# Optimization experiments

Hardware: AMD Instinct MI355X
Metric: run time of the kernel (lower is better)

## Reference

```python
import jax, jax.numpy as jnp
import numpy as np

N_ANGLES = 8
K = 15


def setup_inputs() -> dict:
    key = jax.random.key(0)
    k1, k2, k3 = jax.random.split(key, 3)
    N, Cin, Cout = 2048, 16, 32
    NA = N_ANGLES * N
    x = jax.random.normal(k1, (N, Cin), dtype=jnp.float32)
    # scaled so spectral radius ~1 (like a normalized Laplacian) to keep the
    # Chebyshev recurrence numerically bounded
    Ls = jax.random.normal(k2, (NA, NA), dtype=jnp.float32) / np.float32(np.sqrt(NA))
    fan = N_ANGLES * Cin + Cout  # xavier_uniform bound
    bound = np.float32(np.sqrt(6.0 / fan))
    weight = jax.random.uniform(k3, (K, N_ANGLES * Cin, Cout), dtype=jnp.float32,
                                minval=-bound, maxval=bound)
    bias = jnp.zeros((Cout,), dtype=jnp.float32)
    return {"x": x, "Ls": Ls, "weight": weight, "bias": bias}


def _proj(T, Wk, N, Cin):
    # T: [n_angles*N, Cin] -> [N, n_angles*Cin] @ Wk -> [N, Cout]
    return T.reshape(N_ANGLES, N, Cin).transpose(1, 0, 2).reshape(N, N_ANGLES * Cin) @ Wk


def reference(x, Ls, weight, bias):
    N, Cin = x.shape
    Tx0 = jnp.tile(x, (N_ANGLES, 1))            # [nA*N, Cin]
    out = _proj(Tx0, weight[0], N, Cin)          # [N, Cout]
    Tx1 = Ls @ Tx0
    out = out + _proj(Tx1, weight[1], N, Cin)
    for k in range(2, K):
        Tx2 = 2.0 * (Ls @ Tx1) - Tx0
        out = out + _proj(Tx2, weight[k], N, Cin)
        Tx0, Tx1 = Tx1, Tx2
    return out + bias
```

## Files before the change

### kernel.cpp

```cpp
#include <hip/hip_runtime.h>
#include <hip/hip_fp16.h>

#define NA   16384
#define NN   2048
#define CIN  16
#define COUT 32
#define NANG 8
#define KCH  15
#define NSTEP  512
#define CHUNK  4
#define NCHUNK (NSTEP / CHUNK)
#define NPANEL 1024

#define TSCALE_INV 0.03125f
#define TSCALE     32.0f


typedef _Float16 f16x8 __attribute__((ext_vector_type(8)));
typedef _Float16 f16x4 __attribute__((ext_vector_type(4)));
typedef float    f32x4 __attribute__((ext_vector_type(4)));

__global__ __launch_bounds__(256) void k_tile_t(const float* __restrict__ x,
                                                float* __restrict__ T32,
                                                _Float16* __restrict__ Tsw) {
    int tid = blockIdx.x * 256 + threadIdx.x;
    if (tid >= 8 * 64 * 64) return;
    const int s  = tid >> 12;
    const int st = (tid >> 6) & 63;
    const int l  = tid & 63;
    const int ch = l & 15;
    const int c2 = ((l >> 4) << 3) + (st << 5);
    f16x8 h;
    float v[8];
    #pragma unroll
    for (int e = 0; e < 8; ++e) {
        v[e] = x[(c2 + e) * CIN + ch];
        h[e] = (_Float16)(v[e] * TSCALE_INV);
    }
    float* d = T32 + (size_t)ch * NA + s * (NA / 8) + c2;
    *(float4*)(d)     = make_float4(v[0], v[1], v[2], v[3]);
    *(float4*)(d + 4) = make_float4(v[4], v[5], v[6], v[7]);
    *(f16x8*)(Tsw + (size_t)tid * 8) = h;
}

#define LOADCHUNK(BUF, PC)                                                   \
    _Pragma("unroll")                                                        \
    for (int u = 0; u < CHUNK; ++u) {                                        \
        const int st = (PC) * CHUNK + u;                                     \
        if (CONV) {                                                          \
            f32x4 f0 = __builtin_nontemporal_load((const f32x4*)(aF + (size_t)st * 32));     \
            f32x4 f1 = __builtin_nontemporal_load((const f32x4*)(aF + (size_t)st * 32 + 4)); \
            f16x8 h;                                                         \
            h[0] = (_Float16)f0[0]; h[1] = (_Float16)f0[1];                  \
            h[2] = (_Float16)f0[2]; h[3] = (_Float16)f0[3];                  \
            h[4] = (_Float16)f1[0]; h[5] = (_Float16)f1[1];                  \
            h[6] = (_Float16)f1[2]; h[7] = (_Float16)f1[3];                  \
            __builtin_nontemporal_store(h, (f16x8*)(aW + (size_t)st * 512)); \
            A[BUF][u] = h;                                                   \
        } else {                                                             \
            A[BUF][u] = __builtin_nontemporal_load((const f16x8*)(aP + (size_t)st * 512));   \
        }                                                                    \
        B[BUF][u] = *(const f16x8*)(bP + (size_t)st * 512);                  \
    }

template<int CONV, int REV>
__global__ __launch_bounds__(256)
void k_sweep(const float* __restrict__ Ls,
             _Float16* __restrict__ Lsw,
             const _Float16* __restrict__ Tsw,
             const float* __restrict__ Tp,
             float* __restrict__ Tn,
             _Float16* __restrict__ Tswn,
             float alpha, float beta) {
    constexpr int DEPTH = CONV ? 2 : 4;
    static_assert(NCHUNK % 2 == 0 && NCHUNK % 4 == 0,
                  "tail chunk would replay stale buffer");
    const int w   = threadIdx.x >> 6;
    const int l   = threadIdx.x & 63;
    const int bid = REV ? ((int)gridDim.x - 1 - (int)blockIdx.x) : (int)blockIdx.x;
    const int p   = bid * 4 + w;
    const int rc  = l & 15;
    const int kg  = l >> 4;

    const size_t aoff = (size_t)p * (NSTEP * 512) + (size_t)l * 8;
    const _Float16* aP = Lsw + aoff;
    _Float16*       aW = Lsw + aoff;
    const float*    aF = Ls + (size_t)(p * 16 + rc) * NA + kg * 8;
    const _Float16* bP = Tsw + (size_t)l * 8;

    f32x4 acc = {0.f, 0.f, 0.f, 0.f};
    f16x8 A[DEPTH][CHUNK], B[DEPTH][CHUNK];

    LOADCHUNK(0, 0);
    if (DEPTH >= 3) { LOADCHUNK(1 & (DEPTH - 1), 1); }
    if (DEPTH >= 4) { LOADCHUNK(2 & (DEPTH - 1), 2); }

    #pragma unroll 1
    for (int cc = 0; cc < NCHUNK; cc += DEPTH) {
        #pragma unroll
        for (int d = 0; d < DEPTH; ++d) {
            const int pf = cc + d + DEPTH - 1;
            if (pf < NCHUNK) { LOADCHUNK((d + DEPTH - 1) % DEPTH, pf); }
            #pragma unroll
            for (int u = 0; u < CHUNK; ++u)
                acc = __builtin_amdgcn_mfma_f32_16x16x32_f16(A[d][u], B[d][u],
                                                             acc, 0, 0, 0);
        }
    }

    const size_t tb = (size_t)rc * NA + (size_t)p * 16 + kg * 4;
    float4 tp4 = make_float4(0.f, 0.f, 0.f, 0.f);
    if (beta != 0.f) tp4 = *(const float4*)(Tp + tb);
    const float v0 = alpha * acc[0] + beta * tp4.x;
    const float v1 = alpha * acc[1] + beta * tp4.y;
    const float v2 = alpha * acc[2] + beta * tp4.z;
    const float v3 = alpha * acc[3] + beta * tp4.w;
    *(float4*)(Tn + tb) = make_float4(v0, v1, v2, v3);
    const int c0 = p * 16 + kg * 4;
    const size_t tf = ((size_t)(c0 >> 5) * 64 + ((c0 >> 3) & 3) * 16 + rc) * 8
                      + (c0 & 7);
    f16x4 h;
    h[0] = (_Float16)(v0 * TSCALE_INV); h[1] = (_Float16)(v1 * TSCALE_INV);
    h[2] = (_Float16)(v2 * TSCALE_INV); h[3] = (_Float16)(v3 * TSCALE_INV);
    *(f16x4*)(Tswn + tf) = h;
}

__global__ __launch_bounds__(256) void k_proj_t(const float* __restrict__ Tt,
                                                const float* __restrict__ W,
                                                const float* __restrict__ bias,
                                                float* __restrict__ out, int add) {
    int idx = blockIdx.x * 256 + threadIdx.x;
    if (idx >= NN * COUT) return;
    const int n  = idx >> 5;
    const int co = idx & 31;
    float s = add ? out[idx] : bias[co];
    #pragma unroll
    for (int a = 0; a < NANG; ++a)
        #pragma unroll
        for (int ci = 0; ci < CIN; ++ci)
            s = fmaf(Tt[(size_t)ci * NA + a * NN + n],
                     W[(size_t)(a * CIN + ci) * COUT + co], s);
    out[idx] = s;
}

extern "C" void kernel_launch(void* const* d_in, const int* in_sizes, int n_in,
                              void* d_out, int out_size, void* d_ws, size_t ws_size,
                              hipStream_t stream) {
    const float* x    = (const float*)d_in[0];
    const float* Ls   = (const float*)d_in[1];
    const float* W    = (const float*)d_in[2];
    const float* bias = (const float*)d_in[3];
    float* out = (float*)d_out;

    char* wsb = (char*)d_ws;
    _Float16* Lsw = (_Float16*)wsb;
    float* T32base = (float*)(wsb + (size_t)NA * NA * sizeof(_Float16));
    const size_t TSZ = (size_t)CIN * NA;
    float* T32[3] = { T32base, T32base + TSZ, T32base + 2 * TSZ };
    _Float16* Tswbase = (_Float16*)(T32base + 3 * TSZ);
    _Float16* Tsw[3] = { Tswbase, Tswbase + TSZ, Tswbase + 2 * TSZ };

    const int WSTRIDE = (NANG * CIN) * COUT;
    const int PGRID = (NN * COUT + 255) / 256;
    const int FGRID = (8 * 64 * 64) / 256;
    const int SGRID = NPANEL / 4;

    k_tile_t<<<FGRID, 256, 0, stream>>>(x, T32[0], Tsw[0]);
    k_proj_t<<<PGRID, 256, 0, stream>>>(T32[0], W, bias, out, 0);

    k_sweep<1, 0><<<SGRID, 256, 0, stream>>>(Ls, Lsw, Tsw[0], T32[0],
                                             T32[1], Tsw[1], TSCALE, 0.f);
    k_proj_t<<<PGRID, 256, 0, stream>>>(T32[1], W + WSTRIDE, bias, out, 1);

    int prev = 0, cur = 1;
    for (int k = 2; k < KCH; ++k) {
        int nxt = 3 - cur - prev;
        if (k & 1)
            k_sweep<0, 0><<<SGRID, 256, 0, stream>>>(Ls, Lsw, Tsw[cur], T32[prev],
                                                     T32[nxt], Tsw[nxt],
                                                     2.0f * TSCALE, -1.f);
        else
            k_sweep<0, 1><<<SGRID, 256, 0, stream>>>(Ls, Lsw, Tsw[cur], T32[prev],
                                                     T32[nxt], Tsw[nxt],
                                                     2.0f * TSCALE, -1.f);
        k_proj_t<<<PGRID, 256, 0, stream>>>(T32[nxt], W + (size_t)k * WSTRIDE,
                                            bias, out, 1);
        prev = cur; cur = nxt;
    }
}
```

Baseline: 2.015 ms.

## Fuse previous-step projection into Chebyshev sweep kernel as extra blocks

The projection for step k-1 now runs as extra thread blocks inside the sweep kernel for step k, instead of as a separate launch after each sweep. This removes one kernel launch and its serialization gap per Chebyshev step, and lets the small projection overlap with the memory-bound Ls sweep. The last projection still runs as a standalone launch. The projection blocks are placed first in the grid, so they may delay sweep blocks slightly, and they add register pressure to the sweep kernel.

```diff
diff --git a/kernel.cpp b/kernel.cpp
--- a/kernel.cpp
+++ b/kernel.cpp
@@ -11,6 +11,8 @@
 #define CHUNK  4
 #define NCHUNK (NSTEP / CHUNK)
 #define NPANEL 1024
+#define PGRID  ((NN * COUT) / 256)
+#define SGRID  (NPANEL / 4)
 
 #define TSCALE_INV 0.03125f
 #define TSCALE     32.0f
@@ -41,6 +43,23 @@
     *(float4*)(d)     = make_float4(v[0], v[1], v[2], v[3]);
     *(float4*)(d + 4) = make_float4(v[4], v[5], v[6], v[7]);
     *(f16x8*)(Tsw + (size_t)tid * 8) = h;
+}
+
+__device__ __forceinline__ void proj_body(const float* __restrict__ Tt,
+                                          const float* __restrict__ W,
+                                          const float* __restrict__ bias,
+                                          float* __restrict__ out, int add,
+                                          int idx) {
+    const int n  = idx >> 5;
+    const int co = idx & 31;
+    float s = add ? out[idx] : bias[co];
+    #pragma unroll
+    for (int a = 0; a < NANG; ++a)
+        #pragma unroll
+        for (int ci = 0; ci < CIN; ++ci)
+            s = fmaf(Tt[(size_t)ci * NA + a * NN + n],
+                     W[(size_t)(a * CIN + ci) * COUT + co], s);
+    out[idx] = s;
 }
 
 #define LOADCHUNK(BUF, PC)                                                   \
@@ -71,16 +90,26 @@
              const float* __restrict__ Tp,
              float* __restrict__ Tn,
              _Float16* __restrict__ Tswn,
-             float alpha, float beta) {
+             float alpha, float beta,
+             const float* __restrict__ Tproj,
+             const float* __restrict__ Wk,
+             const float* __restrict__ bias,
+             float* __restrict__ out, int add) {
+    if (blockIdx.x < PGRID) {
+        proj_body(Tproj, Wk, bias, out, add,
+                  (int)blockIdx.x * 256 + (int)threadIdx.x);
+        return;
+    }
     constexpr int DEPTH = CONV ? 2 : 4;
     static_assert(NCHUNK % 2 == 0 && NCHUNK % 4 == 0,
                   "tail chunk would replay stale buffer");
-    const int w   = threadIdx.x >> 6;
-    const int l   = threadIdx.x & 63;
-    const int bid = REV ? ((int)gridDim.x - 1 - (int)blockIdx.x) : (int)blockIdx.x;
-    const int p   = bid * 4 + w;
-    const int rc  = l & 15;
-    const int kg  = l >> 4;
+    const int w    = threadIdx.x >> 6;
+    const int l    = threadIdx.x & 63;
+    const int bid0 = (int)blockIdx.x - PGRID;
+    const int bid  = REV ? (SGRID - 1 - bid0) : bid0;
+    const int p    = bid * 4 + w;
+    const int rc   = l & 15;
+    const int kg   = l >> 4;
 
     const size_t aoff = (size_t)p * (NSTEP * 512) + (size_t)l * 8;
     const _Float16* aP = Lsw + aoff;
@@ -131,16 +160,7 @@
                                                 float* __restrict__ out, int add) {
     int idx = blockIdx.x * 256 + threadIdx.x;
     if (idx >= NN * COUT) return;
-    const int n  = idx >> 5;
-    const int co = idx & 31;
-    float s = add ? out[idx] : bias[co];
-    #pragma unroll
-    for (int a = 0; a < NANG; ++a)
-        #pragma unroll
-        for (int ci = 0; ci < CIN; ++ci)
-            s = fmaf(Tt[(size_t)ci * NA + a * NN + n],
-                     W[(size_t)(a * CIN + ci) * COUT + co], s);
-    out[idx] = s;
+    proj_body(Tt, W, bias, out, add, idx);
 }
 
 extern "C" void kernel_launch(void* const* d_in, const int* in_sizes, int n_in,
@@ -161,30 +181,32 @@
     _Float16* Tsw[3] = { Tswbase, Tswbase + TSZ, Tswbase + 2 * TSZ };
 
     const int WSTRIDE = (NANG * CIN) * COUT;
-    const int PGRID = (NN * COUT + 255) / 256;
     const int FGRID = (8 * 64 * 64) / 256;
-    const int SGRID = NPANEL / 4;
+    const int GRID  = PGRID + SGRID;
 
     k_tile_t<<<FGRID, 256, 0, stream>>>(x, T32[0], Tsw[0]);
-    k_proj_t<<<PGRID, 256, 0, stream>>>(T32[0], W, bias, out, 0);
-
-    k_sweep<1, 0><<<SGRID, 256, 0, stream>>>(Ls, Lsw, Tsw[0], T32[0],
-                                             T32[1], Tsw[1], TSCALE, 0.f);
-    k_proj_t<<<PGRID, 256, 0, stream>>>(T32[1], W + WSTRIDE, bias, out, 1);
+
+    k_sweep<1, 0><<<GRID, 256, 0, stream>>>(Ls, Lsw, Tsw[0], T32[0],
+                                            T32[1], Tsw[1], TSCALE, 0.f,
+                                            T32[0], W, bias, out, 0);
 
     int prev = 0, cur = 1;
     for (int k = 2; k < KCH; ++k) {
         int nxt = 3 - cur - prev;
+        const float* Wk = W + (size_t)(k - 1) * WSTRIDE;
         if (k & 1)
-            k_sweep<0, 0><<<SGRID, 256, 0, stream>>>(Ls, Lsw, Tsw[cur], T32[prev],
-                                                     T32[nxt], Tsw[nxt],
-                                                     2.0f * TSCALE, -1.f);
+            k_sweep<0, 0><<<GRID, 256, 0, stream>>>(Ls, Lsw, Tsw[cur], T32[prev],
+                                                    T32[nxt], Tsw[nxt],
+                                                    2.0f * TSCALE, -1.f,
+                                                    T32[cur], Wk, bias, out, 1);
         else
-            k_sweep<0, 1><<<SGRID, 256, 0, stream>>>(Ls, Lsw, Tsw[cur], T32[prev],
-                                                     T32[nxt], Tsw[nxt],
-                                                     2.0f * TSCALE, -1.f);
-        k_proj_t<<<PGRID, 256, 0, stream>>>(T32[nxt], W + (size_t)k * WSTRIDE,
-                                            bias, out, 1);
+            k_sweep<0, 1><<<GRID, 256, 0, stream>>>(Ls, Lsw, Tsw[cur], T32[prev],
+                                                    T32[nxt], Tsw[nxt],
+                                                    2.0f * TSCALE, -1.f,
+                                                    T32[cur], Wk, bias, out, 1);
         prev = cur; cur = nxt;
     }
-}
+
+    k_proj_t<<<PGRID, 256, 0, stream>>>(T32[cur], W + (size_t)(KCH - 1) * WSTRIDE,
+                                        bias, out, 1);
+}
```

New measurement: 1.686 ms (median of 2 runs). 1.19x faster.
